# Kernel optimization log

Measured on AMD Instinct MI355X. Metric: run time of the kernel, lower is better.

Reference implementation:

```python
import jax, jax.numpy as jnp
import numpy as np

E, HID, T, B, NH, DFF, A, C = 116, 64, 512, 64, 4, 2048, 116, 90


def _ln(x, g, b, eps=1e-5):
    m = x.mean(-1, keepdims=True)
    v = ((x - m) ** 2).mean(-1, keepdims=True)
    return (x - m) / jnp.sqrt(v + eps) * g + b


def _layer(x, p):
    # torch TransformerEncoderLayer, post-norm, relu, eval mode (no dropout)
    wqkv, bqkv, wo, bo, g1, bn1, w1, b1, w2, b2, g2, bn2 = p
    S, N, Em = x.shape  # note: S is the attended axis (dim 0), N the batched axis
    dh = Em // NH
    qkv = x @ wqkv.T + bqkv
    q, k, v = jnp.split(qkv, 3, axis=-1)
    q = q.reshape(S, N, NH, dh)
    k = k.reshape(S, N, NH, dh)
    v = v.reshape(S, N, NH, dh)
    scores = jnp.einsum('snhd,tnhd->nhst', q, k) / np.float32(np.sqrt(dh))
    attn = jax.nn.softmax(scores, axis=-1)
    o = jnp.einsum('nhst,tnhd->snhd', attn, v).reshape(S, N, Em)
    o = o @ wo.T + bo
    x = _ln(x + o, g1, bn1)
    f = jax.nn.relu(x @ w1.T + b1) @ w2.T + b2
    return _ln(x + f, g2, bn2)


def _forward(x, sim, p1, p2, fc_w, fc_b):
    out = _layer(x, p1)
    out1 = _layer(out, p2)
    outs = jnp.transpose(out1, (0, 2, 1))       # (B, E, T)
    fea_ = outs @ fc_w.T + fc_b                 # (B, E, HID)
    feas = jnp.transpose(fea_, (0, 2, 1))       # (B, HID, E)
    fea = feas[:, None, :, :, None]             # (B,1,HID,E,1)
    sim32 = sim.astype(jnp.float32)             # (A, HID, C)
    # cosine_similarity over the HID axis (dim=2 of broadcast tensors),
    # computed without materializing the (B,A,HID,E,C) broadcast product.
    dot = jnp.einsum('bhd,ahc->badc', feas, sim32)           # (B,A,E,C)
    fn = jnp.linalg.norm(feas, axis=1)                       # (B,E)
    sn = jnp.linalg.norm(sim32, axis=1)                      # (A,C)
    denom = jnp.maximum(fn[:, None, :, None] * sn[None, :, None, :], 1e-8)
    similarity = dot / denom                                 # (B,A,E,C)
    similar = similarity.reshape(-1, 116 * 90)
    nrm = jnp.maximum(jnp.linalg.norm(similar, axis=1, keepdims=True), 1e-12)
    similar = similar / nrm
    return fea, similarity, similar


_PNAMES = ['wqkv', 'bqkv', 'wo', 'bo', 'g1', 'bn1', 'w1', 'b1', 'w2', 'b2', 'g2', 'bn2']
_PSHAPES = [(3 * E, E), (3 * E,), (E, E), (E,), (E,), (E,), (DFF, E), (DFF,), (E, DFF), (E,), (E,), (E,)]


def setup_inputs() -> dict:
    key = jax.random.key(0)
    ks = jax.random.split(key, 32)
    s = 0.02
    inp = {
        'x': jax.random.normal(ks[0], (B, T, E), jnp.float32),
        'sim': jax.random.normal(ks[1], (A, HID, C), jnp.float32),
    }
    i = 2
    for L in ('l1', 'l2'):
        for nm, sh in zip(_PNAMES, _PSHAPES):
            if nm in ('g1', 'g2'):
                inp[f'{L}_{nm}'] = jnp.ones(sh, jnp.float32)
            elif nm in ('bqkv', 'bo', 'bn1', 'b1', 'b2', 'bn2'):
                inp[f'{L}_{nm}'] = jnp.zeros(sh, jnp.float32)
            else:
                inp[f'{L}_{nm}'] = jax.random.normal(ks[i], sh, jnp.float32) * s
                i += 1
    inp['fc_w'] = jax.random.normal(ks[i], (HID, T), jnp.float32) * s
    inp['fc_b'] = jnp.zeros((HID,), jnp.float32)
    return inp


def reference(x, sim,
              l1_wqkv, l1_bqkv, l1_wo, l1_bo, l1_g1, l1_bn1, l1_w1, l1_b1, l1_w2, l1_b2, l1_g2, l1_bn2,
              l2_wqkv, l2_bqkv, l2_wo, l2_bo, l2_g1, l2_bn1, l2_w1, l2_b1, l2_w2, l2_b2, l2_g2, l2_bn2,
              fc_w, fc_b):
    p1 = (l1_wqkv, l1_bqkv, l1_wo, l1_bo, l1_g1, l1_bn1, l1_w1, l1_b1, l1_w2, l1_b2, l1_g2, l1_bn2)
    p2 = (l2_wqkv, l2_bqkv, l2_wo, l2_bo, l2_g1, l2_bn1, l2_w1, l2_b1, l2_w2, l2_b2, l2_g2, l2_bn2)
    return _forward(x, sim, p1, p2, fc_w, fc_b)
```

## Files before the change

kernel.cpp:

```cpp
#include <hip/hip_runtime.h>
#include <hip/hip_bf16.h>

typedef __attribute__((ext_vector_type(8))) short short8v;
typedef __attribute__((ext_vector_type(4))) float floatx4;

__device__ __forceinline__ float bf2f(unsigned short u) {
  union { unsigned int i; float f; } c;
  c.i = ((unsigned int)u) << 16;
  return c.f;
}
__device__ __forceinline__ unsigned short f2bf(float f) {
  __hip_bfloat16 h = __float2bfloat16(f);
  return *reinterpret_cast<unsigned short*>(&h);
}

struct ConvJobs {
  const float* src[9];
  unsigned short* dst[9];
  int K[9];
  int Kp[9];
  int mode[9];
  int cum[10];
};

__global__ __launch_bounds__(256) void convert_all_kernel(ConvJobs J) {
  const int total = J.cum[9];
  for (int idx = blockIdx.x * 256 + threadIdx.x; idx < total;
       idx += gridDim.x * 256) {
    int j = 0;
    while (idx >= J.cum[j + 1]) ++j;
    const int local = idx - J.cum[j];
    const int Kp = J.Kp[j];
    const int r = local / Kp, c = local - r * Kp;
    unsigned short v;
    if (J.mode[j] == 0) {
      v = (c < J.K[j]) ? f2bf(J.src[j][(size_t)r * J.K[j] + c])
                       : (unsigned short)0;
    } else {
      const int h = c >> 5, d = c & 31;
      v = (d < 29) ? f2bf(J.src[j][(size_t)r * 116 + h * 29 + d])
                   : (unsigned short)0;
    }
    J.dst[j][local] = v;
  }
}

__global__ __launch_bounds__(256) void qkv_gemm_kernel(
    const unsigned short* __restrict__ A,
    const unsigned short* __restrict__ B,
    const float* __restrict__ bias,
    unsigned short* __restrict__ qkvp) {
  __shared__ __align__(16) unsigned char shmem[32768];
  unsigned short (*As)[64] = reinterpret_cast<unsigned short(*)[64]>(shmem);
  unsigned short (*Bs)[64] =
      reinterpret_cast<unsigned short(*)[64]>(shmem + 16384);
  unsigned short (*Qt)[120] = reinterpret_cast<unsigned short(*)[120]>(shmem);

  const int tid = threadIdx.x;
  const int M0 = blockIdx.x * 128;
  const int which = blockIdx.y;
  const int wid = tid >> 6, lane = tid & 63;
  const int wr = wid >> 1, wc = wid & 1;
  const int lc = lane & 15, g = lane >> 4;
  const int srow = tid >> 1, shalf = tid & 1;
  const int sw = srow & 7;

  floatx4 acc[4][4] = {};

  for (int kt = 0; kt < 2; ++kt) {
    const int k0 = kt << 6;
    {
      const uint4* p = reinterpret_cast<const uint4*>(
          A + (size_t)(M0 + srow) * 128 + k0 + shalf * 32);
      uint4 v0 = p[0], v1 = p[1], v2 = p[2], v3 = p[3];
      *reinterpret_cast<uint4*>(&As[srow][((((shalf << 2) | 0) ^ sw) << 3)]) = v0;
      *reinterpret_cast<uint4*>(&As[srow][((((shalf << 2) | 1) ^ sw) << 3)]) = v1;
      *reinterpret_cast<uint4*>(&As[srow][((((shalf << 2) | 2) ^ sw) << 3)]) = v2;
      *reinterpret_cast<uint4*>(&As[srow][((((shalf << 2) | 3) ^ sw) << 3)]) = v3;
    }
    {
      uint4 v0 = {0, 0, 0, 0}, v1 = v0, v2 = v0, v3 = v0;
      if (srow < 116) {
        const uint4* p = reinterpret_cast<const uint4*>(
            B + (size_t)(which * 116 + srow) * 128 + k0 + shalf * 32);
        v0 = p[0]; v1 = p[1]; v2 = p[2]; v3 = p[3];
      }
      *reinterpret_cast<uint4*>(&Bs[srow][((((shalf << 2) | 0) ^ sw) << 3)]) = v0;
      *reinterpret_cast<uint4*>(&Bs[srow][((((shalf << 2) | 1) ^ sw) << 3)]) = v1;
      *reinterpret_cast<uint4*>(&Bs[srow][((((shalf << 2) | 2) ^ sw) << 3)]) = v2;
      *reinterpret_cast<uint4*>(&Bs[srow][((((shalf << 2) | 3) ^ sw) << 3)]) = v3;
    }
    __syncthreads();
#pragma unroll
    for (int ks = 0; ks < 2; ++ks) {
      short8v a[4], b[4];
#pragma unroll
      for (int m = 0; m < 4; ++m) {
        const int row = wr * 64 + m * 16 + lc;
        a[m] = *reinterpret_cast<const short8v*>(
            &As[row][((((ks << 2) | g) ^ (lc & 7)) << 3)]);
      }
#pragma unroll
      for (int n = 0; n < 4; ++n) {
        const int col = wc * 64 + n * 16 + lc;
        b[n] = *reinterpret_cast<const short8v*>(
            &Bs[col][((((ks << 2) | g) ^ (lc & 7)) << 3)]);
      }
#pragma unroll
      for (int m = 0; m < 4; ++m)
#pragma unroll
        for (int n = 0; n < 4; ++n)
          acc[m][n] = __builtin_amdgcn_mfma_f32_16x16x32_bf16(a[m], b[n],
                                                              acc[m][n], 0, 0, 0);
    }
    __syncthreads();
  }

#pragma unroll
  for (int m = 0; m < 4; ++m) {
#pragma unroll
    for (int r = 0; r < 4; ++r) {
      const int lrow = wr * 64 + m * 16 + g * 4 + r;
#pragma unroll
      for (int n = 0; n < 4; ++n) {
        const int col = wc * 64 + n * 16 + lc;
        if (col < 116)
          Qt[lrow][col] = f2bf(acc[m][n][r] + bias[which * 116 + col]);
      }
    }
  }
  __syncthreads();

  const int s_idx = M0 >> 9;
  const int nbase = M0 & 511;
  for (int idx = tid; idx < 2048; idx += 256) {
    const int dg = idx & 3, h = (idx >> 2) & 3, n = idx >> 4;
    unsigned short ow[8];
#pragma unroll
    for (int j = 0; j < 8; ++j) {
      const int d = dg * 8 + j;
      ow[j] = (d < 29) ? Qt[n][h * 29 + d] : (unsigned short)0;
    }
    uint4* dst = reinterpret_cast<uint4*>(
        qkvp + (size_t)which * 4194304 +
        ((((size_t)(nbase + n) * 4 + h) * 64 + s_idx) << 5) + dg * 8);
    *dst = *reinterpret_cast<const uint4*>(ow);
  }
}

__global__ __launch_bounds__(256) void mgemm64_ln_kernel(
    const unsigned short* __restrict__ A, const unsigned short* __restrict__ B,
    const float* __restrict__ bias, int Kp, unsigned short* __restrict__ Yb,
    float* __restrict__ Yf, const float* __restrict__ res,
    const float* __restrict__ gw, const float* __restrict__ bw) {
  __shared__ __align__(16) unsigned short As[64][64];
  __shared__ __align__(16) unsigned short Bs[128][64];
  __shared__ float sum1[2][64];
  __shared__ float sum2[2][64];

  const int tid = threadIdx.x;
  const int M0 = blockIdx.x * 64;
  const int wid = tid >> 6, lane = tid & 63;
  const int wr = wid >> 1, wc = wid & 1;
  const int lc = lane & 15, g = lane >> 4;
  const int arow = tid >> 2, aq = tid & 3;
  const int brow = tid >> 1, bhalf = tid & 1;

  floatx4 acc[2][4] = {};

  const int nk = Kp >> 6;
  for (int kt = 0; kt < nk; ++kt) {
    const int k0 = kt << 6;
    {
      const uint4* p = reinterpret_cast<const uint4*>(
          A + (size_t)(M0 + arow) * Kp + k0 + aq * 16);
      uint4 v0 = p[0], v1 = p[1];
      const int swa = arow & 7;
      *reinterpret_cast<uint4*>(&As[arow][(((aq * 2) ^ swa) << 3)]) = v0;
      *reinterpret_cast<uint4*>(&As[arow][(((aq * 2 + 1) ^ swa) << 3)]) = v1;
    }
    {
      uint4 v0 = {0, 0, 0, 0}, v1 = v0, v2 = v0, v3 = v0;
      if (brow < 116) {
        const uint4* p = reinterpret_cast<const uint4*>(
            B + (size_t)brow * Kp + k0 + bhalf * 32);
        v0 = p[0]; v1 = p[1]; v2 = p[2]; v3 = p[3];
      }
      const int sw = brow & 7;
      *reinterpret_cast<uint4*>(&Bs[brow][((((bhalf << 2) | 0) ^ sw) << 3)]) = v0;
      *reinterpret_cast<uint4*>(&Bs[brow][((((bhalf << 2) | 1) ^ sw) << 3)]) = v1;
      *reinterpret_cast<uint4*>(&Bs[brow][((((bhalf << 2) | 2) ^ sw) << 3)]) = v2;
      *reinterpret_cast<uint4*>(&Bs[brow][((((bhalf << 2) | 3) ^ sw) << 3)]) = v3;
    }
    __syncthreads();
#pragma unroll
    for (int ks = 0; ks < 2; ++ks) {
      short8v a[2], b[4];
#pragma unroll
      for (int m = 0; m < 2; ++m) {
        const int row = wr * 32 + m * 16 + lc;
        a[m] = *reinterpret_cast<const short8v*>(
            &As[row][((((ks << 2) | g) ^ (row & 7)) << 3)]);
      }
#pragma unroll
      for (int n = 0; n < 4; ++n) {
        const int col = wc * 64 + n * 16 + lc;
        b[n] = *reinterpret_cast<const short8v*>(
            &Bs[col][((((ks << 2) | g) ^ (col & 7)) << 3)]);
      }
#pragma unroll
      for (int m = 0; m < 2; ++m)
#pragma unroll
        for (int n = 0; n < 4; ++n)
          acc[m][n] = __builtin_amdgcn_mfma_f32_16x16x32_bf16(a[m], b[n],
                                                              acc[m][n], 0, 0, 0);
    }
    __syncthreads();
  }

  float s1l[2][4], s2l[2][4];
#pragma unroll
  for (int m = 0; m < 2; ++m) {
#pragma unroll
    for (int r = 0; r < 4; ++r) {
      const int row = M0 + wr * 32 + m * 16 + g * 4 + r;
      float s = 0.f, s2 = 0.f;
#pragma unroll
      for (int n = 0; n < 4; ++n) {
        const int col = wc * 64 + n * 16 + lc;
        float v = 0.f;
        if (col < 116)
          v = acc[m][n][r] + bias[col] + res[(size_t)row * 116 + col];
        acc[m][n][r] = v;
        s += v;
        s2 = fmaf(v, v, s2);
      }
#pragma unroll
      for (int st = 1; st < 16; st <<= 1) {
        s += __shfl_xor(s, st, 16);
        s2 += __shfl_xor(s2, st, 16);
      }
      s1l[m][r] = s;
      s2l[m][r] = s2;
    }
  }
  if (lc == 0) {
#pragma unroll
    for (int m = 0; m < 2; ++m)
#pragma unroll
      for (int r = 0; r < 4; ++r) {
        const int lrow = wr * 32 + m * 16 + g * 4 + r;
        sum1[wc][lrow] = s1l[m][r];
        sum2[wc][lrow] = s2l[m][r];
      }
  }
  __syncthreads();
#pragma unroll
  for (int m = 0; m < 2; ++m) {
#pragma unroll
    for (int r = 0; r < 4; ++r) {
      const int lrow = wr * 32 + m * 16 + g * 4 + r;
      const int row = M0 + lrow;
      const float st = sum1[0][lrow] + sum1[1][lrow];
      const float s2t = sum2[0][lrow] + sum2[1][lrow];
      const float mean = st * (1.f / 116.f);
      const float var = s2t * (1.f / 116.f) - mean * mean;
      const float rstd = 1.f / sqrtf(var + 1e-5f);
#pragma unroll
      for (int n = 0; n < 4; ++n) {
        const int col = wc * 64 + n * 16 + lc;
        if (col < 116) {
          const float y = (acc[m][n][r] - mean) * rstd * gw[col] + bw[col];
          Yf[(size_t)row * 116 + col] = y;
          Yb[(size_t)row * 128 + col] = f2bf(y);
        } else {
          Yb[(size_t)row * 128 + col] = 0;
        }
      }
    }
  }
}

__global__ __launch_bounds__(512, 1) void ffn_fused2_kernel(
    const unsigned short* __restrict__ Xa,
    const unsigned short* __restrict__ W1,
    const float* __restrict__ b1,
    const unsigned short* __restrict__ W2,
    const float* __restrict__ b2, const float* __restrict__ res,
    const float* __restrict__ gw, const float* __restrict__ bw,
    unsigned short* __restrict__ Yb,
    float* __restrict__ Yf) {
  __shared__ __align__(16) unsigned short Xs[128][128];
  __shared__ __align__(16) unsigned short W1c[128][128];
  __shared__ __align__(16) unsigned short W2c[128][128];
  __shared__ __align__(16) unsigned short Hs[128][136];
  __shared__ float sum1[2][128];
  __shared__ float sum2[2][128];

  const int tid = threadIdx.x;
  const int M0 = blockIdx.x * 128;
  const int wid = tid >> 6, lane = tid & 63;
  const int wtr = wid >> 1, wdc = wid & 1;
  const int lc = lane & 15, g = lane >> 4;
  const int srow = tid >> 2, aq = tid & 3;

  {
    const uint4* p = reinterpret_cast<const uint4*>(
        Xa + (size_t)(M0 + srow) * 128 + aq * 32);
#pragma unroll
    for (int q = 0; q < 4; ++q) {
      const int cj = aq * 4 + q;
      const int swz = (cj & 8) | ((cj ^ srow) & 7);
      *reinterpret_cast<uint4*>(&Xs[srow][swz * 8]) = p[q];
    }
  }

  uint4 w1r[4], w2r[4];
  {
    const uint4* p1 =
        reinterpret_cast<const uint4*>(W1 + (size_t)srow * 128 + aq * 32);
#pragma unroll
    for (int q = 0; q < 4; ++q) w1r[q] = p1[q];
    uint4 z = {0, 0, 0, 0};
    w2r[0] = z; w2r[1] = z; w2r[2] = z; w2r[3] = z;
    if (srow < 116) {
      const uint4* p2 =
          reinterpret_cast<const uint4*>(W2 + (size_t)srow * 2048 + aq * 32);
#pragma unroll
      for (int q = 0; q < 4; ++q) w2r[q] = p2[q];
    }
  }

  floatx4 oacc[2][4] = {};

  for (int kc = 0; kc < 16; ++kc) {
#pragma unroll
    for (int q = 0; q < 4; ++q) {
      const int cj = aq * 4 + q;
      const int swz = (cj & 8) | ((cj ^ srow) & 7);
      *reinterpret_cast<uint4*>(&W1c[srow][swz * 8]) = w1r[q];
      *reinterpret_cast<uint4*>(&W2c[srow][swz * 8]) = w2r[q];
    }
    if (kc < 15) {
      const uint4* p1 = reinterpret_cast<const uint4*>(
          W1 + (size_t)((kc + 1) * 128 + srow) * 128 + aq * 32);
#pragma unroll
      for (int q = 0; q < 4; ++q) w1r[q] = p1[q];
      if (srow < 116) {
        const uint4* p2 = reinterpret_cast<const uint4*>(
            W2 + (size_t)srow * 2048 + (kc + 1) * 128 + aq * 32);
#pragma unroll
        for (int q = 0; q < 4; ++q) w2r[q] = p2[q];
      }
    }
    __syncthreads();

    floatx4 hacc[2][4] = {};
#pragma unroll
    for (int ks = 0; ks < 4; ++ks) {
      short8v av[2], bv[4];
      const int cj = ks * 4 + g;
#pragma unroll
      for (int m = 0; m < 2; ++m) {
        const int row = wtr * 32 + m * 16 + lc;
        const int swz = (cj & 8) | ((cj ^ row) & 7);
        av[m] = *reinterpret_cast<const short8v*>(&Xs[row][swz * 8]);
      }
#pragma unroll
      for (int n = 0; n < 4; ++n) {
        const int row = wdc * 64 + n * 16 + lc;
        const int swz = (cj & 8) | ((cj ^ row) & 7);
        bv[n] = *reinterpret_cast<const short8v*>(&W1c[row][swz * 8]);
      }
#pragma unroll
      for (int m = 0; m < 2; ++m)
#pragma unroll
        for (int n = 0; n < 4; ++n)
          hacc[m][n] = __builtin_amdgcn_mfma_f32_16x16x32_bf16(av[m], bv[n],
                                                               hacc[m][n], 0, 0, 0);
    }
#pragma unroll
    for (int n = 0; n < 4; ++n) {
      const int dff = wdc * 64 + n * 16 + lc;
      const float bb = b1[kc * 128 + dff];
#pragma unroll
      for (int m = 0; m < 2; ++m) {
#pragma unroll
        for (int r = 0; r < 4; ++r) {
          const int tok = wtr * 32 + m * 16 + g * 4 + r;
          Hs[tok][dff] = f2bf(fmaxf(hacc[m][n][r] + bb, 0.f));
        }
      }
    }
    __syncthreads();

#pragma unroll
    for (int ks = 0; ks < 4; ++ks) {
      short8v av[2], bv[4];
      const int cj = ks * 4 + g;
#pragma unroll
      for (int m = 0; m < 2; ++m) {
        const int row = wtr * 32 + m * 16 + lc;
        av[m] = *reinterpret_cast<const short8v*>(&Hs[row][cj * 8]);
      }
#pragma unroll
      for (int n = 0; n < 4; ++n) {
        const int col = wdc * 64 + n * 16 + lc;
        const int swz = (cj & 8) | ((cj ^ col) & 7);
        bv[n] = *reinterpret_cast<const short8v*>(&W2c[col][swz * 8]);
      }
#pragma unroll
      for (int m = 0; m < 2; ++m)
#pragma unroll
        for (int n = 0; n < 4; ++n)
          oacc[m][n] = __builtin_amdgcn_mfma_f32_16x16x32_bf16(av[m], bv[n],
                                                               oacc[m][n], 0, 0, 0);
    }
    __syncthreads();
  }

  float s1l[2][4], s2l[2][4];
#pragma unroll
  for (int m = 0; m < 2; ++m) {
#pragma unroll
    for (int r = 0; r < 4; ++r) {
      const int row = M0 + wtr * 32 + m * 16 + g * 4 + r;
      float s = 0.f, s2 = 0.f;
#pragma unroll
      for (int n = 0; n < 4; ++n) {
        const int col = wdc * 64 + n * 16 + lc;
        float v = 0.f;
        if (col < 116)
          v = oacc[m][n][r] + b2[col] + res[(size_t)row * 116 + col];
        oacc[m][n][r] = v;
        s += v;
        s2 = fmaf(v, v, s2);
      }
#pragma unroll
      for (int st = 1; st < 16; st <<= 1) {
        s += __shfl_xor(s, st, 16);
        s2 += __shfl_xor(s2, st, 16);
      }
      s1l[m][r] = s;
      s2l[m][r] = s2;
    }
  }
  if (lc == 0) {
#pragma unroll
    for (int m = 0; m < 2; ++m)
#pragma unroll
      for (int r = 0; r < 4; ++r) {
        const int lrow = wtr * 32 + m * 16 + g * 4 + r;
        sum1[wdc][lrow] = s1l[m][r];
        sum2[wdc][lrow] = s2l[m][r];
      }
  }
  __syncthreads();
#pragma unroll
  for (int m = 0; m < 2; ++m) {
#pragma unroll
    for (int r = 0; r < 4; ++r) {
      const int lrow = wtr * 32 + m * 16 + g * 4 + r;
      const int row = M0 + lrow;
      const float st = sum1[0][lrow] + sum1[1][lrow];
      const float s2t = sum2[0][lrow] + sum2[1][lrow];
      const float mean = st * (1.f / 116.f);
      const float var = s2t * (1.f / 116.f) - mean * mean;
      const float rstd = 1.f / sqrtf(var + 1e-5f);
#pragma unroll
      for (int n = 0; n < 4; ++n) {
        const int col = wdc * 64 + n * 16 + lc;
        if (col < 116) {
          const float y = (oacc[m][n][r] - mean) * rstd * gw[col] + bw[col];
          Yf[(size_t)row * 116 + col] = y;
          Yb[(size_t)row * 128 + col] = f2bf(y);
        } else {
          Yb[(size_t)row * 128 + col] = 0;
        }
      }
    }
  }
}

__global__ __launch_bounds__(64) void attn_kernel(
    const unsigned short* __restrict__ qkvp, unsigned short* __restrict__ obuf) {
  const int h = blockIdx.x & 3;
  const int n = blockIdx.x >> 2;
  const int s = threadIdx.x;
  __shared__ float ks[64][36];
  __shared__ float vs[64][36];

  const size_t rb = (((size_t)n * 4 + h) * 64 + s) * 32;
  const uint4* qp = reinterpret_cast<const uint4*>(qkvp + rb);
  const uint4* kp = reinterpret_cast<const uint4*>(qkvp + 4194304 + rb);
  const uint4* vp = reinterpret_cast<const uint4*>(qkvp + 8388608 + rb);
  uint4 qv[4], kv4[4], vv4[4];
#pragma unroll
  for (int i = 0; i < 4; ++i) {
    qv[i] = qp[i];
    kv4[i] = kp[i];
    vv4[i] = vp[i];
  }
  float q[32], kf[32], vf[32];
#pragma unroll
  for (int i = 0; i < 4; ++i) {
    const unsigned* wq = reinterpret_cast<const unsigned*>(&qv[i]);
    const unsigned* wk = reinterpret_cast<const unsigned*>(&kv4[i]);
    const unsigned* wv = reinterpret_cast<const unsigned*>(&vv4[i]);
#pragma unroll
    for (int j = 0; j < 4; ++j) {
      union { unsigned u; float f; } lo, hi;
      const int d0 = i * 8 + 2 * j;
      lo.u = wq[j] << 16; hi.u = wq[j] & 0xffff0000u;
      q[d0] = lo.f; q[d0 + 1] = hi.f;
      lo.u = wk[j] << 16; hi.u = wk[j] & 0xffff0000u;
      kf[d0] = (d0 < 29) ? lo.f : 0.f;
      kf[d0 + 1] = (d0 + 1 < 29) ? hi.f : 0.f;
      lo.u = wv[j] << 16; hi.u = wv[j] & 0xffff0000u;
      vf[d0] = (d0 < 29) ? lo.f : 0.f;
      vf[d0 + 1] = (d0 + 1 < 29) ? hi.f : 0.f;
    }
  }
  q[29] = q[30] = q[31] = 0.f;
#pragma unroll
  for (int c = 0; c < 8; ++c) {
    *reinterpret_cast<float4*>(&ks[s][c * 4]) =
        make_float4(kf[4 * c], kf[4 * c + 1], kf[4 * c + 2], kf[4 * c + 3]);
    *reinterpret_cast<float4*>(&vs[s][c * 4]) =
        make_float4(vf[4 * c], vf[4 * c + 1], vf[4 * c + 2], vf[4 * c + 3]);
  }
  __syncthreads();

  const float scale = 0.18569533817705186f;
  float sc[64];
#pragma unroll 4
  for (int t = 0; t < 64; ++t) {
    const float4* kr = reinterpret_cast<const float4*>(&ks[t][0]);
    float a = 0.f;
#pragma unroll
    for (int c = 0; c < 8; ++c) {
      const float4 kc = kr[c];
      a = fmaf(q[4 * c], kc.x, a);
      a = fmaf(q[4 * c + 1], kc.y, a);
      a = fmaf(q[4 * c + 2], kc.z, a);
      a = fmaf(q[4 * c + 3], kc.w, a);
    }
    sc[t] = a * scale;
  }
  float m = sc[0];
#pragma unroll
  for (int t = 1; t < 64; ++t) m = fmaxf(m, sc[t]);
  float sum = 0.f;
#pragma unroll
  for (int t = 0; t < 64; ++t) {
    sc[t] = __expf(sc[t] - m);
    sum += sc[t];
  }
  const float inv = 1.f / sum;
  float o[32] = {};
#pragma unroll 4
  for (int t = 0; t < 64; ++t) {
    const float p = sc[t];
    const float4* vr = reinterpret_cast<const float4*>(&vs[t][0]);
#pragma unroll
    for (int c = 0; c < 8; ++c) {
      const float4 vc = vr[c];
      o[4 * c] = fmaf(p, vc.x, o[4 * c]);
      o[4 * c + 1] = fmaf(p, vc.y, o[4 * c + 1]);
      o[4 * c + 2] = fmaf(p, vc.z, o[4 * c + 2]);
      o[4 * c + 3] = fmaf(p, vc.w, o[4 * c + 3]);
    }
  }
  unsigned short ow[32];
#pragma unroll
  for (int i = 0; i < 32; ++i) ow[i] = f2bf(o[i] * inv);
  uint4* od =
      reinterpret_cast<uint4*>(obuf + ((size_t)s * 512 + n) * 128 + h * 32);
  const uint4* ows = reinterpret_cast<const uint4*>(ow);
#pragma unroll
  for (int i = 0; i < 4; ++i) od[i] = ows[i];
}

__global__ __launch_bounds__(256) void fc_kernel(
    const float* __restrict__ X4, const float* __restrict__ fw,
    const float* __restrict__ fb, float* __restrict__ fea,
    unsigned short* __restrict__ feaT, float* __restrict__ fn) {
  const int eg = blockIdx.x;
  const int b = blockIdx.y;
  const int e0 = eg * 29;
  __shared__ float Os[64][30];
  __shared__ float Wf[64][65];
  const int tid = threadIdx.x;
  const int h = tid & 63, jg = tid >> 6;
  float acc[8] = {};

  for (int tc = 0; tc < 8; ++tc) {
    for (int idx = tid; idx < 64 * 29; idx += 256) {
      int tt = idx / 29;
      int ee = idx - tt * 29;
      Os[tt][ee] = X4[((size_t)b * 512 + tc * 64 + tt) * 116 + e0 + ee];
    }
    for (int idx = tid; idx < 64 * 64; idx += 256) {
      int hh = idx >> 6, t2 = idx & 63;
      Wf[hh][t2] = fw[(size_t)hh * 512 + tc * 64 + t2];
    }
    __syncthreads();
#pragma unroll 4
    for (int t = 0; t < 64; ++t) {
      const float w = Wf[h][t];
#pragma unroll
      for (int m = 0; m < 8; ++m) {
        const int el = jg + 4 * m;
        if (el < 29) acc[m] = fmaf(Os[t][el], w, acc[m]);
      }
    }
    __syncthreads();
  }
  const float bb = fb[h];
#pragma unroll
  for (int m = 0; m < 8; ++m) {
    const int el = jg + 4 * m;
    if (el < 29) {
      const float v = acc[m] + bb;
      const int e = e0 + el;
      fea[((size_t)b * 64 + h) * 116 + e] = v;
      if (feaT) {
        const unsigned short vb = f2bf(v);
        feaT[((size_t)b * 128 + e) * 64 + h] = vb;
        float s = bf2f(vb);
        s = s * s;
#pragma unroll
        for (int st = 1; st <= 32; st <<= 1) s += __shfl_xor(s, st, 64);
        if (h == 0) fn[b * 128 + e] = sqrtf(s);
      }
    }
  }
}

__global__ __launch_bounds__(256) void simt_prep_kernel(
    const float* __restrict__ simin, unsigned short* __restrict__ simT,
    float* __restrict__ sn) {
  __shared__ float L[64][91];
  const int a = blockIdx.x;
  const int tid = threadIdx.x;
  for (int idx = tid; idx < 64 * 90; idx += 256) {
    const int h = idx / 90, c = idx - h * 90;
    L[h][c] = bf2f(f2bf(simin[((size_t)a * 64 + h) * 90 + c]));
  }
  __syncthreads();
  for (int idx = tid; idx < 96 * 64; idx += 256) {
    const int c = idx >> 6, h = idx & 63;
    simT[((size_t)a * 96 + c) * 64 + h] = (c < 90) ? f2bf(L[h][c]) : 0;
  }
  if (tid < 90) {
    float s = 0.f;
#pragma unroll 8
    for (int h = 0; h < 64; ++h) {
      const float t = L[h][tid];
      s = fmaf(t, t, s);
    }
    sn[a * 96 + tid] = sqrtf(s);
  }
}

__global__ __launch_bounds__(256) void sim_mfma3_kernel(
    const unsigned short* __restrict__ feaT, const unsigned short* __restrict__ simT,
    const float* __restrict__ fn, const float* __restrict__ sn,
    float* __restrict__ simil, float* __restrict__ similar) {
  const int a0 = blockIdx.x * 4;
  const int b = blockIdx.y;
  __shared__ __align__(16) unsigned short Ft[128][64];
  __shared__ __align__(16) unsigned short St[96][64];
  __shared__ __align__(16) float Rs[10440];
  __shared__ float fnrow[116];
  __shared__ float snrow[90];
  __shared__ float wred[4];
  const int tid = threadIdx.x;
  const int srow = tid >> 1, shalf = tid & 1;
  const int sw = srow & 7;
  const int wid = tid >> 6, lane = tid & 63;
  const int wr = wid >> 1, wc = wid & 1;
  const int lc = lane & 15, g = lane >> 4;

  {
    const uint4* p = reinterpret_cast<const uint4*>(
        feaT + ((size_t)b * 128 + srow) * 64 + shalf * 32);
    uint4 v0 = p[0], v1 = p[1], v2 = p[2], v3 = p[3];
    *reinterpret_cast<uint4*>(&Ft[srow][((((shalf << 2) | 0) ^ sw) << 3)]) = v0;
    *reinterpret_cast<uint4*>(&Ft[srow][((((shalf << 2) | 1) ^ sw) << 3)]) = v1;
    *reinterpret_cast<uint4*>(&Ft[srow][((((shalf << 2) | 2) ^ sw) << 3)]) = v2;
    *reinterpret_cast<uint4*>(&Ft[srow][((((shalf << 2) | 3) ^ sw) << 3)]) = v3;
  }
  if (tid < 116) fnrow[tid] = fn[b * 128 + tid];

  for (int ai = 0; ai < 4; ++ai) {
    const int a = a0 + ai;
    if (srow < 96) {
      const uint4* p = reinterpret_cast<const uint4*>(
          simT + ((size_t)a * 96 + srow) * 64 + shalf * 32);
      uint4 v0 = p[0], v1 = p[1], v2 = p[2], v3 = p[3];
      *reinterpret_cast<uint4*>(&St[srow][((((shalf << 2) | 0) ^ sw) << 3)]) = v0;
      *reinterpret_cast<uint4*>(&St[srow][((((shalf << 2) | 1) ^ sw) << 3)]) = v1;
      *reinterpret_cast<uint4*>(&St[srow][((((shalf << 2) | 2) ^ sw) << 3)]) = v2;
      *reinterpret_cast<uint4*>(&St[srow][((((shalf << 2) | 3) ^ sw) << 3)]) = v3;
    }
    if (tid >= 160 && tid < 250) snrow[tid - 160] = sn[a * 96 + (tid - 160)];
    __syncthreads();

    floatx4 acc[4][3] = {};
#pragma unroll
    for (int ks = 0; ks < 2; ++ks) {
      short8v av[4], bv[3];
#pragma unroll
      for (int m = 0; m < 4; ++m) {
        const int row = wr * 64 + m * 16 + lc;
        av[m] = *reinterpret_cast<const short8v*>(
            &Ft[row][((((ks << 2) | g) ^ (lc & 7)) << 3)]);
      }
#pragma unroll
      for (int n = 0; n < 3; ++n) {
        const int col = wc * 48 + n * 16 + lc;
        bv[n] = *reinterpret_cast<const short8v*>(
            &St[col][((((ks << 2) | g) ^ (lc & 7)) << 3)]);
      }
#pragma unroll
      for (int m = 0; m < 4; ++m)
#pragma unroll
        for (int n = 0; n < 3; ++n)
          acc[m][n] = __builtin_amdgcn_mfma_f32_16x16x32_bf16(av[m], bv[n],
                                                              acc[m][n], 0, 0, 0);
    }

    float ss = 0.f;
#pragma unroll
    for (int m = 0; m < 4; ++m) {
#pragma unroll
      for (int r = 0; r < 4; ++r) {
        const int d = wr * 64 + m * 16 + g * 4 + r;
        if (d < 116) {
          const float fnv = fnrow[d];
#pragma unroll
          for (int n = 0; n < 3; ++n) {
            const int c = wc * 48 + n * 16 + lc;
            if (c < 90) {
              const float denom = fmaxf(fnv * snrow[c], 1e-8f);
              float rcp = __builtin_amdgcn_rcpf(denom);
              rcp = rcp * (2.0f - denom * rcp);
              const float v = acc[m][n][r] * rcp;
              ss = fmaf(v, v, ss);
              Rs[d * 90 + c] = v;
            }
          }
        }
      }
    }
#pragma unroll
    for (int st = 1; st <= 32; st <<= 1) ss += __shfl_xor(ss, st, 64);
    if (lane == 0) wred[wid] = ss;
    __syncthreads();
    const float tot = wred[0] + wred[1] + wred[2] + wred[3];
    const float inv = 1.f / fmaxf(sqrtf(tot), 1e-12f);

    const size_t rowbase = ((size_t)b * 116 + a) * (116 * 90);
    float4* so = reinterpret_cast<float4*>(simil + rowbase);
    float4* sr = reinterpret_cast<float4*>(similar + rowbase);
    const float4* rs4 = reinterpret_cast<const float4*>(Rs);
    for (int i = tid; i < 2610; i += 256) {
      float4 v = rs4[i];
      so[i] = v;
      float4 w;
      w.x = v.x * inv; w.y = v.y * inv; w.z = v.z * inv; w.w = v.w * inv;
      sr[i] = w;
    }
  }
}

__global__ __launch_bounds__(256) void sim_mfma_kernel(
    const float* __restrict__ fea, const float* __restrict__ simin,
    float* __restrict__ simil, float* __restrict__ similar) {
  const int a = blockIdx.x;
  const int b = blockIdx.y;
  __shared__ __align__(16) unsigned char shmem[41760];
  __shared__ float fnrow[116];
  __shared__ float snrow[90];
  __shared__ float wred[4];
  const int tid = threadIdx.x;

  unsigned short (*Ft)[64] = reinterpret_cast<unsigned short(*)[64]>(shmem);
  unsigned short (*St)[64] =
      reinterpret_cast<unsigned short(*)[64]>(shmem + 16384);
  float* Rs = reinterpret_cast<float*>(shmem);

  for (int idx = tid; idx < 64 * 116; idx += 256) {
    const int h = idx / 116, d = idx - h * 116;
    Ft[d][(((h >> 3) ^ (d & 7)) << 3) | (h & 7)] =
        f2bf(fea[((size_t)b * 64 + h) * 116 + d]);
  }
  for (int idx = tid; idx < 12 * 64; idx += 256) {
    const int d = 116 + (idx >> 6), h = idx & 63;
    Ft[d][(((h >> 3) ^ (d & 7)) << 3) | (h & 7)] = 0;
  }
  for (int idx = tid; idx < 64 * 90; idx += 256) {
    const int h = idx / 90, c = idx - h * 90;
    St[c][(((h >> 3) ^ (c & 7)) << 3) | (h & 7)] =
        f2bf(simin[((size_t)a * 64 + h) * 90 + c]);
  }
  for (int idx = tid; idx < 6 * 64; idx += 256) {
    const int c = 90 + (idx >> 6), h = idx & 63;
    St[c][(((h >> 3) ^ (c & 7)) << 3) | (h & 7)] = 0;
  }
  __syncthreads();

  if (tid < 116) {
    float s = 0.f;
#pragma unroll 8
    for (int h = 0; h < 64; ++h) {
      const float t = bf2f(Ft[tid][(((h >> 3) ^ (tid & 7)) << 3) | (h & 7)]);
      s = fmaf(t, t, s);
    }
    fnrow[tid] = sqrtf(s);
  } else if (tid >= 128 && tid < 218) {
    const int c = tid - 128;
    float s = 0.f;
#pragma unroll 8
    for (int h = 0; h < 64; ++h) {
      const float t = bf2f(St[c][(((h >> 3) ^ (c & 7)) << 3) | (h & 7)]);
      s = fmaf(t, t, s);
    }
    snrow[c] = sqrtf(s);
  }
  __syncthreads();

  const int wid = tid >> 6, lane = tid & 63;
  const int wr = wid >> 1, wc = wid & 1;
  const int lc = lane & 15, g = lane >> 4;

  floatx4 acc[4][3] = {};
#pragma unroll
  for (int ks = 0; ks < 2; ++ks) {
    short8v av[4], bv[3];
#pragma unroll
    for (int m = 0; m < 4; ++m) {
      const int row = wr * 64 + m * 16 + lc;
      av[m] = *reinterpret_cast<const short8v*>(
          &Ft[row][((((ks << 2) | g) ^ (lc & 7)) << 3)]);
    }
#pragma unroll
    for (int n = 0; n < 3; ++n) {
      const int col = wc * 48 + n * 16 + lc;
      bv[n] = *reinterpret_cast<const short8v*>(
          &St[col][((((ks << 2) | g) ^ (lc & 7)) << 3)]);
    }
#pragma unroll
    for (int m = 0; m < 4; ++m)
#pragma unroll
      for (int n = 0; n < 3; ++n)
        acc[m][n] = __builtin_amdgcn_mfma_f32_16x16x32_bf16(av[m], bv[n],
                                                            acc[m][n], 0, 0, 0);
  }
  __syncthreads();

  float ss = 0.f;
#pragma unroll
  for (int m = 0; m < 4; ++m) {
#pragma unroll
    for (int r = 0; r < 4; ++r) {
      const int d = wr * 64 + m * 16 + g * 4 + r;
      if (d < 116) {
        const float fnv = fnrow[d];
#pragma unroll
        for (int n = 0; n < 3; ++n) {
          const int c = wc * 48 + n * 16 + lc;
          if (c < 90) {
            const float denom = fmaxf(fnv * snrow[c], 1e-8f);
            float rcp = __builtin_amdgcn_rcpf(denom);
            rcp = rcp * (2.0f - denom * rcp);
            const float v = acc[m][n][r] * rcp;
            ss = fmaf(v, v, ss);
            Rs[d * 90 + c] = v;
          }
        }
      }
    }
  }
#pragma unroll
  for (int st = 1; st <= 32; st <<= 1) ss += __shfl_xor(ss, st, 64);
  if (lane == 0) wred[wid] = ss;
  __syncthreads();
  const float tot = wred[0] + wred[1] + wred[2] + wred[3];
  const float inv = 1.f / fmaxf(sqrtf(tot), 1e-12f);

  const size_t rowbase = ((size_t)b * 116 + a) * (116 * 90);
  float4* so = reinterpret_cast<float4*>(simil + rowbase);
  float4* sr = reinterpret_cast<float4*>(similar + rowbase);
  const float4* rs4 = reinterpret_cast<const float4*>(Rs);
  for (int i = tid; i < 2610; i += 256) {
    float4 v = rs4[i];
    so[i] = v;
    float4 w;
    w.x = v.x * inv; w.y = v.y * inv; w.z = v.z * inv; w.w = v.w * inv;
    sr[i] = w;
  }
}

extern "C" void kernel_launch(void* const* d_in, const int* in_sizes, int n_in,
                              void* d_out, int out_size, void* d_ws,
                              size_t ws_size, hipStream_t stream) {
  const float* x0 = (const float*)d_in[0];
  const float* simin = (const float*)d_in[1];
  const float* p[24];
  for (int i = 0; i < 24; ++i) p[i] = (const float*)d_in[2 + i];
  const float* fc_w = (const float*)d_in[26];
  const float* fc_b = (const float*)d_in[27];

  float* out = (float*)d_out;
  float* fea = out;
  float* simil = out + 475136;
  float* similar = out + 77981696;

  float* xa_f[2] = {similar + 0, similar + 7602176};
  float* xb_f[2] = {similar + 3801088, similar + 11403264};
  unsigned short* obufb = (unsigned short*)(similar + 15204352);
  unsigned short* qkvp = (unsigned short*)(similar + 17301504);
  unsigned short* Ab = (unsigned short*)(similar + 23592960);
  unsigned short* xab[2] = {(unsigned short*)(similar + 25690112),
                            (unsigned short*)(similar + 29884416)};
  unsigned short* xbb[2] = {(unsigned short*)(similar + 27787264),
                            (unsigned short*)(similar + 31981568)};
  unsigned short* wbuf = (unsigned short*)(simil + 33554432);
  const size_t WSZ = 559104;

  unsigned char* ws = (unsigned char*)d_ws;
  unsigned short* feaT = (unsigned short*)ws;
  unsigned short* simT = (unsigned short*)(ws + 1048576);
  float* fnb = (float*)(ws + 2473984);
  float* snb = (float*)(ws + 2506752);
  const bool ws_ok = ws_size >= 2551296;

  {
    ConvJobs J;
    int cum = 0;
    auto add = [&](int j, const float* s, unsigned short* dd, int R, int K,
                   int Kp, int mode) {
      J.src[j] = s; J.dst[j] = dd; J.K[j] = K; J.Kp[j] = Kp; J.mode[j] = mode;
      J.cum[j] = cum; cum += R * Kp;
    };
    add(0, x0, Ab, 32768, 116, 128, 0);
    for (int L = 0; L < 2; ++L) {
      unsigned short* wb = wbuf + L * WSZ;
      add(1 + L * 4, p[L * 12 + 0], wb + 0, 348, 116, 128, 0);
      add(2 + L * 4, p[L * 12 + 2], wb + 44544, 116, 116, 128, 1);
      add(3 + L * 4, p[L * 12 + 6], wb + 59392, 2048, 116, 128, 0);
      add(4 + L * 4, p[L * 12 + 8], wb + 321536, 116, 2048, 2048, 0);
    }
    J.cum[9] = cum;
    hipLaunchKernelGGL(convert_all_kernel, dim3(2048), dim3(256), 0, stream, J);
  }

  if (ws_ok) {
    hipLaunchKernelGGL(simt_prep_kernel, dim3(116), dim3(256), 0, stream,
                       simin, simT, snb);
  }

  const unsigned short* Ain = Ab;
  const float* resin = x0;
  for (int L = 0; L < 2; ++L) {
    unsigned short* wb = wbuf + L * WSZ;
    const float* bqkv = p[L * 12 + 1];
    const float* bo = p[L * 12 + 3];
    const float* g1 = p[L * 12 + 4];
    const float* bn1 = p[L * 12 + 5];
    const float* b1 = p[L * 12 + 7];
    const float* b2 = p[L * 12 + 9];
    const float* g2 = p[L * 12 + 10];
    const float* bn2 = p[L * 12 + 11];

    hipLaunchKernelGGL(qkv_gemm_kernel, dim3(256, 3), dim3(256), 0, stream,
                       Ain, wb + 0, bqkv, qkvp);
    hipLaunchKernelGGL(attn_kernel, dim3(2048), dim3(64), 0, stream, qkvp,
                       obufb);
    hipLaunchKernelGGL(mgemm64_ln_kernel, dim3(512), dim3(256), 0, stream,
                       obufb, wb + 44544, bo, 128, xab[L], xa_f[L], resin, g1,
                       bn1);
    hipLaunchKernelGGL(ffn_fused2_kernel, dim3(256), dim3(512), 0, stream,
                       xab[L], wb + 59392, b1, wb + 321536, b2, xa_f[L], g2,
                       bn2, xbb[L], xb_f[L]);
    Ain = xbb[L];
    resin = xb_f[L];
  }

  if (ws_ok) {
    hipLaunchKernelGGL(fc_kernel, dim3(4, 64), dim3(256), 0, stream, xb_f[1],
                       fc_w, fc_b, fea, feaT, fnb);
    hipLaunchKernelGGL(sim_mfma3_kernel, dim3(29, 64), dim3(256), 0, stream,
                       feaT, simT, fnb, snb, simil, similar);
  } else {
    hipLaunchKernelGGL(fc_kernel, dim3(4, 64), dim3(256), 0, stream, xb_f[1],
                       fc_w, fc_b, fea, (unsigned short*)nullptr,
                       (float*)nullptr);
    hipLaunchKernelGGL(sim_mfma_kernel, dim3(116, 64), dim3(256), 0, stream,
                       fea, simin, simil, similar);
  }
}
```

Measured before the change: 606.3 us.

## Read FFN weights directly from global memory and halve the row tile per block

The fused FFN kernel no longer stages W1/W2 chunks through LDS with register prefetch. Each wave now loads its MFMA B-operands straight from global memory, which is expected to hit in cache. The block shrinks to 64 tokens and 256 threads with two blocks per CU, launched as 512 blocks, which cuts LDS use and removes the per-chunk sync for weight staging. The cost is uncoalesced 16-byte global loads sitting in the MFMA inner loop, and weight traffic through cache is duplicated across more blocks.

```diff
diff --git a/kernel.cpp b/kernel.cpp
--- a/kernel.cpp
+++ b/kernel.cpp
@@ -281,7 +281,7 @@
   }
 }
 
-__global__ __launch_bounds__(512, 1) void ffn_fused2_kernel(
+__global__ __launch_bounds__(256, 2) void ffn_fused4_kernel(
     const unsigned short* __restrict__ Xa,
     const unsigned short* __restrict__ W1,
     const float* __restrict__ b1,
@@ -290,71 +290,33 @@
     const float* __restrict__ gw, const float* __restrict__ bw,
     unsigned short* __restrict__ Yb,
     float* __restrict__ Yf) {
-  __shared__ __align__(16) unsigned short Xs[128][128];
-  __shared__ __align__(16) unsigned short W1c[128][128];
-  __shared__ __align__(16) unsigned short W2c[128][128];
-  __shared__ __align__(16) unsigned short Hs[128][136];
-  __shared__ float sum1[2][128];
-  __shared__ float sum2[2][128];
+  __shared__ __align__(16) unsigned short Xs[64][128];
+  __shared__ __align__(16) unsigned short Hs[64][136];
+  __shared__ float sum1[2][64];
+  __shared__ float sum2[2][64];
 
   const int tid = threadIdx.x;
-  const int M0 = blockIdx.x * 128;
+  const int M0 = blockIdx.x * 64;
   const int wid = tid >> 6, lane = tid & 63;
-  const int wtr = wid >> 1, wdc = wid & 1;
+  const int wr = wid >> 1, wc = wid & 1;
   const int lc = lane & 15, g = lane >> 4;
-  const int srow = tid >> 2, aq = tid & 3;
+  const int arow = tid >> 2, aq = tid & 3;
 
   {
     const uint4* p = reinterpret_cast<const uint4*>(
-        Xa + (size_t)(M0 + srow) * 128 + aq * 32);
+        Xa + (size_t)(M0 + arow) * 128 + aq * 32);
 #pragma unroll
     for (int q = 0; q < 4; ++q) {
       const int cj = aq * 4 + q;
-      const int swz = (cj & 8) | ((cj ^ srow) & 7);
-      *reinterpret_cast<uint4*>(&Xs[srow][swz * 8]) = p[q];
-    }
-  }
-
-  uint4 w1r[4], w2r[4];
-  {
-    const uint4* p1 =
-        reinterpret_cast<const uint4*>(W1 + (size_t)srow * 128 + aq * 32);
-#pragma unroll
-    for (int q = 0; q < 4; ++q) w1r[q] = p1[q];
-    uint4 z = {0, 0, 0, 0};
-    w2r[0] = z; w2r[1] = z; w2r[2] = z; w2r[3] = z;
-    if (srow < 116) {
-      const uint4* p2 =
-          reinterpret_cast<const uint4*>(W2 + (size_t)srow * 2048 + aq * 32);
-#pragma unroll
-      for (int q = 0; q < 4; ++q) w2r[q] = p2[q];
-    }
-  }
+      const int swz = (cj & 8) | ((cj ^ arow) & 7);
+      *reinterpret_cast<uint4*>(&Xs[arow][swz * 8]) = p[q];
+    }
+  }
+  __syncthreads();
 
   floatx4 oacc[2][4] = {};
 
   for (int kc = 0; kc < 16; ++kc) {
-#pragma unroll
-    for (int q = 0; q < 4; ++q) {
-      const int cj = aq * 4 + q;
-      const int swz = (cj & 8) | ((cj ^ srow) & 7);
-      *reinterpret_cast<uint4*>(&W1c[srow][swz * 8]) = w1r[q];
-      *reinterpret_cast<uint4*>(&W2c[srow][swz * 8]) = w2r[q];
-    }
-    if (kc < 15) {
-      const uint4* p1 = reinterpret_cast<const uint4*>(
-          W1 + (size_t)((kc + 1) * 128 + srow) * 128 + aq * 32);
-#pragma unroll
-      for (int q = 0; q < 4; ++q) w1r[q] = p1[q];
-      if (srow < 116) {
-        const uint4* p2 = reinterpret_cast<const uint4*>(
-            W2 + (size_t)srow * 2048 + (kc + 1) * 128 + aq * 32);
-#pragma unroll
-        for (int q = 0; q < 4; ++q) w2r[q] = p2[q];
-      }
-    }
-    __syncthreads();
-
     floatx4 hacc[2][4] = {};
 #pragma unroll
     for (int ks = 0; ks < 4; ++ks) {
@@ -362,15 +324,15 @@
       const int cj = ks * 4 + g;
 #pragma unroll
       for (int m = 0; m < 2; ++m) {
-        const int row = wtr * 32 + m * 16 + lc;
+        const int row = wr * 32 + m * 16 + lc;
         const int swz = (cj & 8) | ((cj ^ row) & 7);
         av[m] = *reinterpret_cast<const short8v*>(&Xs[row][swz * 8]);
       }
 #pragma unroll
       for (int n = 0; n < 4; ++n) {
-        const int row = wdc * 64 + n * 16 + lc;
-        const int swz = (cj & 8) | ((cj ^ row) & 7);
-        bv[n] = *reinterpret_cast<const short8v*>(&W1c[row][swz * 8]);
+        const int dffrow = kc * 128 + wc * 64 + n * 16 + lc;
+        bv[n] = *reinterpret_cast<const short8v*>(
+            W1 + (size_t)dffrow * 128 + ks * 32 + g * 8);
       }
 #pragma unroll
       for (int m = 0; m < 2; ++m)
@@ -381,13 +343,13 @@
     }
 #pragma unroll
     for (int n = 0; n < 4; ++n) {
-      const int dff = wdc * 64 + n * 16 + lc;
+      const int dff = wc * 64 + n * 16 + lc;
       const float bb = b1[kc * 128 + dff];
 #pragma unroll
       for (int m = 0; m < 2; ++m) {
 #pragma unroll
         for (int r = 0; r < 4; ++r) {
-          const int tok = wtr * 32 + m * 16 + g * 4 + r;
+          const int tok = wr * 32 + m * 16 + g * 4 + r;
           Hs[tok][dff] = f2bf(fmaxf(hacc[m][n][r] + bb, 0.f));
         }
       }
@@ -400,14 +362,18 @@
       const int cj = ks * 4 + g;
 #pragma unroll
       for (int m = 0; m < 2; ++m) {
-        const int row = wtr * 32 + m * 16 + lc;
+        const int row = wr * 32 + m * 16 + lc;
         av[m] = *reinterpret_cast<const short8v*>(&Hs[row][cj * 8]);
       }
 #pragma unroll
       for (int n = 0; n < 4; ++n) {
-        const int col = wdc * 64 + n * 16 + lc;
-        const int swz = (cj & 8) | ((cj ^ col) & 7);
-        bv[n] = *reinterpret_cast<const short8v*>(&W2c[col][swz * 8]);
+        const int e = wc * 64 + n * 16 + lc;
+        if (e < 116) {
+          bv[n] = *reinterpret_cast<const short8v*>(
+              W2 + (size_t)e * 2048 + kc * 128 + ks * 32 + g * 8);
+        } else {
+          bv[n] = short8v{0, 0, 0, 0, 0, 0, 0, 0};
+        }
       }
 #pragma unroll
       for (int m = 0; m < 2; ++m)
@@ -424,11 +390,11 @@
   for (int m = 0; m < 2; ++m) {
 #pragma unroll
     for (int r = 0; r < 4; ++r) {
-      const int row = M0 + wtr * 32 + m * 16 + g * 4 + r;
+      const int row = M0 + wr * 32 + m * 16 + g * 4 + r;
       float s = 0.f, s2 = 0.f;
 #pragma unroll
       for (int n = 0; n < 4; ++n) {
-        const int col = wdc * 64 + n * 16 + lc;
+        const int col = wc * 64 + n * 16 + lc;
         float v = 0.f;
         if (col < 116)
           v = oacc[m][n][r] + b2[col] + res[(size_t)row * 116 + col];
@@ -450,9 +416,9 @@
     for (int m = 0; m < 2; ++m)
 #pragma unroll
       for (int r = 0; r < 4; ++r) {
-        const int lrow = wtr * 32 + m * 16 + g * 4 + r;
-        sum1[wdc][lrow] = s1l[m][r];
-        sum2[wdc][lrow] = s2l[m][r];
+        const int lrow = wr * 32 + m * 16 + g * 4 + r;
+        sum1[wc][lrow] = s1l[m][r];
+        sum2[wc][lrow] = s2l[m][r];
       }
   }
   __syncthreads();
@@ -460,7 +426,7 @@
   for (int m = 0; m < 2; ++m) {
 #pragma unroll
     for (int r = 0; r < 4; ++r) {
-      const int lrow = wtr * 32 + m * 16 + g * 4 + r;
+      const int lrow = wr * 32 + m * 16 + g * 4 + r;
       const int row = M0 + lrow;
       const float st = sum1[0][lrow] + sum1[1][lrow];
       const float s2t = sum2[0][lrow] + sum2[1][lrow];
@@ -469,7 +435,7 @@
       const float rstd = 1.f / sqrtf(var + 1e-5f);
 #pragma unroll
       for (int n = 0; n < 4; ++n) {
-        const int col = wdc * 64 + n * 16 + lc;
+        const int col = wc * 64 + n * 16 + lc;
         if (col < 116) {
           const float y = (oacc[m][n][r] - mean) * rstd * gw[col] + bw[col];
           Yf[(size_t)row * 116 + col] = y;
@@ -982,7 +948,7 @@
     hipLaunchKernelGGL(mgemm64_ln_kernel, dim3(512), dim3(256), 0, stream,
                        obufb, wb + 44544, bo, 128, xab[L], xa_f[L], resin, g1,
                        bn1);
-    hipLaunchKernelGGL(ffn_fused2_kernel, dim3(256), dim3(512), 0, stream,
+    hipLaunchKernelGGL(ffn_fused4_kernel, dim3(512), dim3(256), 0, stream,
                        xab[L], wb + 59392, b1, wb + 321536, b2, xa_f[L], g2,
                        bn2, xbb[L], xb_f[L]);
     Ain = xbb[L];
```

Result: slower. 704.5 us (+16.2%).
